# Performance work log

Hardware: AMD Instinct MI355X
Metric: run time of the kernel (lower is better)

## Reference

```python
import jax, jax.numpy as jnp
import numpy as np

NUM_NODES = 100000
EMBED_DIM = 128
NUM_RELATIONS = 64
BATCH = 512


def setup_inputs() -> dict:
    key = jax.random.key(0)
    k1, k2, k3, k4, k5 = jax.random.split(key, 5)
    u = jax.random.randint(k1, (BATCH,), 0, NUM_NODES)
    v = jax.random.randint(k2, (BATCH,), 0, NUM_NODES)
    r = jax.random.randint(k3, (BATCH,), 0, NUM_RELATIONS)
    node_embeddings = jax.random.normal(k4, (NUM_NODES, EMBED_DIM), dtype=jnp.float32)
    relation_matrices = jax.random.normal(k5, (NUM_RELATIONS, EMBED_DIM, EMBED_DIM), dtype=jnp.float32)
    return {"u": u, "v": v, "r": r,
            "node_embeddings": node_embeddings,
            "relation_matrices": relation_matrices}


def reference(u, v, r, node_embeddings, relation_matrices):
    u_embed = node_embeddings[u]            # [B, D]
    v_embed = node_embeddings[v]            # [B, D]
    rel = relation_matrices[r]              # [B, D, D] per-sample gathered matrices
    # torch.matmul([B,D], [B,D,D]) broadcasts u_embed over the relation batch -> [B_rel, B_u, D]
    score = jnp.einsum('ud,bde->bue', u_embed, rel)   # [B, B, D]
    # matmul with v_embed.T [D, B] -> [B, B, B]
    score = jnp.einsum('bue,ve->buv', score, v_embed)  # [B, B, B]
    return jax.nn.sigmoid(score)
```

## Files before the change

kernel.cpp:

```cpp
#include <hip/hip_runtime.h>


#define BATCH 512
#define DIM   128
#define NRELS 64
#define NTHR  256

typedef float floatx4 __attribute__((ext_vector_type(4)));

#define T_ELEMS   ((size_t)NRELS * DIM * BATCH)
#define CNT_OFF   (T_ELEMS)
#define LIST_OFF  (T_ELEMS + 64)
#define WS_NEED   ((T_ELEMS + 64 + (size_t)NRELS * BATCH) * 4)

__global__ __launch_bounds__(NTHR, 2)
void rad_prep_kernel(const int* __restrict__ u_idx,
                     const int* __restrict__ r_idx,
                     const float* __restrict__ nodes,
                     const float* __restrict__ rels,
                     float* __restrict__ ws)
{
    const int bid = (int)blockIdx.x;
    const int t   = (int)threadIdx.x;

    if (bid == NRELS * 8) {
        __shared__ int s_cnt[NRELS];
        int* counts = (int*)(ws + CNT_OFF);
        int* lists  = (int*)(ws + LIST_OFF);
        if (t < NRELS) s_cnt[t] = 0;
        __syncthreads();
        for (int i = t; i < BATCH; i += NTHR) {
            const int rel = r_idx[i];
            const int pos = atomicAdd(&s_cnt[rel], 1);
            lists[rel * BATCH + pos] = i;
        }
        __syncthreads();
        if (t < NRELS) counts[t] = s_cnt[t];
        return;
    }

    const int rel = bid >> 3;
    const int ut0 = (bid & 7) * 64;

    __shared__ __align__(16) float UEsT[DIM * 64];
    __shared__ __align__(16) float Rs[16 * DIM];

    const int tu = t >> 4;
    const int tx = t & 15;

    for (int i = t; i < 64 * (DIM / 4); i += NTHR) {
        const int row = i & 63;
        const int dc  = i >> 6;
        const float4 val = *reinterpret_cast<const float4*>(
            nodes + (size_t)u_idx[ut0 + row] * DIM + dc * 4);
        UEsT[(dc * 4 + 0) * 64 + row] = val.x;
        UEsT[(dc * 4 + 1) * 64 + row] = val.y;
        UEsT[(dc * 4 + 2) * 64 + row] = val.z;
        UEsT[(dc * 4 + 3) * 64 + row] = val.w;
    }

    float accA[4][8];
    #pragma unroll
    for (int i = 0; i < 4; ++i)
        #pragma unroll
        for (int j = 0; j < 8; ++j) accA[i][j] = 0.f;

    const float* Rbase = rels + (size_t)rel * DIM * DIM;
    for (int dch = 0; dch < DIM / 16; ++dch) {
        __syncthreads();
        for (int i = t; i < 16 * (DIM / 4); i += NTHR) {
            const int rr = i >> 5;
            const int cc = i & 31;
            *reinterpret_cast<float4*>(Rs + rr * DIM + cc * 4) =
                *reinterpret_cast<const float4*>(
                    Rbase + (size_t)(dch * 16 + rr) * DIM + cc * 4);
        }
        __syncthreads();
        #pragma unroll
        for (int dd = 0; dd < 16; ++dd) {
            const int d = dch * 16 + dd;
            const float4 a  = *reinterpret_cast<const float4*>(UEsT + d * 64 + tu * 4);
            const float4 b0 = *reinterpret_cast<const float4*>(Rs + dd * DIM + tx * 4);
            const float4 b1 = *reinterpret_cast<const float4*>(Rs + dd * DIM + 64 + tx * 4);
            const float av[4] = {a.x, a.y, a.z, a.w};
            const float bv[8] = {b0.x, b0.y, b0.z, b0.w, b1.x, b1.y, b1.z, b1.w};
            #pragma unroll
            for (int i = 0; i < 4; ++i)
                #pragma unroll
                for (int j = 0; j < 8; ++j)
                    accA[i][j] = fmaf(av[i], bv[j], accA[i][j]);
        }
    }

    #pragma unroll
    for (int j = 0; j < 8; ++j) {
        const int e = (j < 4) ? (tx * 4 + j) : (64 + tx * 4 + (j - 4));
        float4 w4 = make_float4(accA[0][j], accA[1][j], accA[2][j], accA[3][j]);
        *reinterpret_cast<float4*>(
            ws + ((size_t)rel * DIM + e) * BATCH + ut0 + tu * 4) = w4;
    }
}

__global__ __launch_bounds__(NTHR, 2)
void rad_tile_kernel(const int* __restrict__ v_idx,
                     const float* __restrict__ nodes,
                     const float* __restrict__ ws,
                     float* __restrict__ out)
{
    const int bid = (int)blockIdx.x;
    const int rel = bid >> 6;
    const int ut0 = ((bid >> 3) & 7) * 64;
    const int vt0 = (bid & 7) * 64;

    const int* counts = (const int*)(ws + CNT_OFF);
    const int* lists  = (const int*)(ws + LIST_OFF) + rel * BATCH;
    const int  mc     = counts[rel];
    if (mc == 0) return;

    __shared__ __align__(16) float TsT[DIM * 64];
    __shared__ __align__(16) float VEsT[DIM * 64];

    const int t  = (int)threadIdx.x;
    const int tu = t >> 4;
    const int tx = t & 15;

    const float* Tbase = ws + (size_t)rel * DIM * BATCH + ut0;
    for (int i = t; i < DIM * 16; i += NTHR) {
        const int e  = i >> 4;
        const int uc = i & 15;
        *reinterpret_cast<float4*>(TsT + e * 64 + uc * 4) =
            *reinterpret_cast<const float4*>(Tbase + (size_t)e * BATCH + uc * 4);
    }
    for (int i = t; i < 64 * (DIM / 4); i += NTHR) {
        const int row = i & 63;
        const int ec  = i >> 6;
        const float4 val = *reinterpret_cast<const float4*>(
            nodes + (size_t)v_idx[vt0 + row] * DIM + ec * 4);
        VEsT[(ec * 4 + 0) * 64 + row] = val.x;
        VEsT[(ec * 4 + 1) * 64 + row] = val.y;
        VEsT[(ec * 4 + 2) * 64 + row] = val.z;
        VEsT[(ec * 4 + 3) * 64 + row] = val.w;
    }
    __syncthreads();

    float acc[4][4];
    #pragma unroll
    for (int i = 0; i < 4; ++i)
        #pragma unroll
        for (int j = 0; j < 4; ++j) acc[i][j] = 0.f;

    #pragma unroll 8
    for (int e = 0; e < DIM; ++e) {
        const float4 a = *reinterpret_cast<const float4*>(TsT  + e * 64 + tu * 4);
        const float4 b = *reinterpret_cast<const float4*>(VEsT + e * 64 + tx * 4);
        const float av[4] = {a.x, a.y, a.z, a.w};
        const float bv[4] = {b.x, b.y, b.z, b.w};
        #pragma unroll
        for (int i = 0; i < 4; ++i)
            #pragma unroll
            for (int j = 0; j < 4; ++j)
                acc[i][j] = fmaf(av[i], bv[j], acc[i][j]);
    }

    floatx4 sg[4];
    #pragma unroll
    for (int i = 0; i < 4; ++i) {
        sg[i].x = 1.f / (1.f + __expf(-acc[i][0]));
        sg[i].y = 1.f / (1.f + __expf(-acc[i][1]));
        sg[i].z = 1.f / (1.f + __expf(-acc[i][2]));
        sg[i].w = 1.f / (1.f + __expf(-acc[i][3]));
    }

    for (int m = 0; m < mc; ++m) {
        const int bb = lists[m];
        float* obase = out + (size_t)bb * BATCH * BATCH + vt0 + tx * 4;
        #pragma unroll
        for (int i = 0; i < 4; ++i) {
            __builtin_nontemporal_store(
                sg[i], reinterpret_cast<floatx4*>(
                           obase + (size_t)(ut0 + tu * 4 + i) * BATCH));
        }
    }
}

__global__ __launch_bounds__(NTHR, 2)
void rad_fused_kernel(const int* __restrict__ u_idx,
                      const int* __restrict__ v_idx,
                      const int* __restrict__ r_idx,
                      const float* __restrict__ nodes,
                      const float* __restrict__ rels,
                      float* __restrict__ out)
{
    const int rel = (int)blockIdx.x >> 3;
    const int ut0 = ((int)blockIdx.x & 7) * 64;

    __shared__ int s_match[BATCH];
    __shared__ int s_mc;
    __shared__ __align__(16) float s_TsT[DIM * 64];
    __shared__ __align__(16) float s_buf[DIM * 64 + 16 * DIM];

    const int t  = (int)threadIdx.x;
    const int tu = t >> 4;
    const int tx = t & 15;

    if (t == 0) s_mc = 0;
    __syncthreads();
    for (int i = t; i < BATCH; i += NTHR) {
        if (r_idx[i] == rel) {
            int p = atomicAdd(&s_mc, 1);
            s_match[p] = i;
        }
    }

    float* UEsT = s_buf;
    float* Rs   = s_buf + DIM * 64;

    for (int i = t; i < 64 * (DIM / 4); i += NTHR) {
        const int row = i & 63;
        const int dc  = i >> 6;
        const float4 val = *reinterpret_cast<const float4*>(
            nodes + (size_t)u_idx[ut0 + row] * DIM + dc * 4);
        UEsT[(dc * 4 + 0) * 64 + row] = val.x;
        UEsT[(dc * 4 + 1) * 64 + row] = val.y;
        UEsT[(dc * 4 + 2) * 64 + row] = val.z;
        UEsT[(dc * 4 + 3) * 64 + row] = val.w;
    }
    __syncthreads();
    const int mc = s_mc;
    if (mc == 0) return;

    float accA[4][8];
    #pragma unroll
    for (int i = 0; i < 4; ++i)
        #pragma unroll
        for (int j = 0; j < 8; ++j) accA[i][j] = 0.f;

    const float* Rbase = rels + (size_t)rel * DIM * DIM;
    for (int dch = 0; dch < DIM / 16; ++dch) {
        for (int i = t; i < 16 * (DIM / 4); i += NTHR) {
            const int rr = i >> 5;
            const int cc = i & 31;
            *reinterpret_cast<float4*>(Rs + rr * DIM + cc * 4) =
                *reinterpret_cast<const float4*>(
                    Rbase + (size_t)(dch * 16 + rr) * DIM + cc * 4);
        }
        __syncthreads();
        #pragma unroll
        for (int dd = 0; dd < 16; ++dd) {
            const int d = dch * 16 + dd;
            const float4 a  = *reinterpret_cast<const float4*>(UEsT + d * 64 + tu * 4);
            const float4 b0 = *reinterpret_cast<const float4*>(Rs + dd * DIM + tx * 4);
            const float4 b1 = *reinterpret_cast<const float4*>(Rs + dd * DIM + 64 + tx * 4);
            const float av[4] = {a.x, a.y, a.z, a.w};
            const float bv[8] = {b0.x, b0.y, b0.z, b0.w, b1.x, b1.y, b1.z, b1.w};
            #pragma unroll
            for (int i = 0; i < 4; ++i)
                #pragma unroll
                for (int j = 0; j < 8; ++j)
                    accA[i][j] = fmaf(av[i], bv[j], accA[i][j]);
        }
        __syncthreads();
    }

    #pragma unroll
    for (int j = 0; j < 8; ++j) {
        const int e = (j < 4) ? (tx * 4 + j) : (64 + tx * 4 + (j - 4));
        #pragma unroll
        for (int i = 0; i < 4; ++i)
            s_TsT[e * 64 + tu * 4 + i] = accA[i][j];
    }

    float* VEsT = s_buf;
    for (int vt = 0; vt < BATCH / 64; ++vt) {
        __syncthreads();
        for (int i = t; i < 64 * (DIM / 4); i += NTHR) {
            const int row = i & 63;
            const int ec  = i >> 6;
            const float4 val = *reinterpret_cast<const float4*>(
                nodes + (size_t)v_idx[vt * 64 + row] * DIM + ec * 4);
            VEsT[(ec * 4 + 0) * 64 + row] = val.x;
            VEsT[(ec * 4 + 1) * 64 + row] = val.y;
            VEsT[(ec * 4 + 2) * 64 + row] = val.z;
            VEsT[(ec * 4 + 3) * 64 + row] = val.w;
        }
        __syncthreads();

        float acc[4][4];
        #pragma unroll
        for (int i = 0; i < 4; ++i)
            #pragma unroll
            for (int j = 0; j < 4; ++j) acc[i][j] = 0.f;

        #pragma unroll 8
        for (int e = 0; e < DIM; ++e) {
            const float4 a = *reinterpret_cast<const float4*>(s_TsT + e * 64 + tu * 4);
            const float4 b = *reinterpret_cast<const float4*>(VEsT  + e * 64 + tx * 4);
            const float av[4] = {a.x, a.y, a.z, a.w};
            const float bv[4] = {b.x, b.y, b.z, b.w};
            #pragma unroll
            for (int i = 0; i < 4; ++i)
                #pragma unroll
                for (int j = 0; j < 4; ++j)
                    acc[i][j] = fmaf(av[i], bv[j], acc[i][j]);
        }

        floatx4 sg[4];
        #pragma unroll
        for (int i = 0; i < 4; ++i) {
            sg[i].x = 1.f / (1.f + __expf(-acc[i][0]));
            sg[i].y = 1.f / (1.f + __expf(-acc[i][1]));
            sg[i].z = 1.f / (1.f + __expf(-acc[i][2]));
            sg[i].w = 1.f / (1.f + __expf(-acc[i][3]));
        }

        for (int m = 0; m < mc; ++m) {
            const int bb = s_match[m];
            float* obase = out + (size_t)bb * BATCH * BATCH;
            #pragma unroll
            for (int i = 0; i < 4; ++i) {
                floatx4* dst = reinterpret_cast<floatx4*>(
                    obase + (size_t)(ut0 + tu * 4 + i) * BATCH + vt * 64 + tx * 4);
                __builtin_nontemporal_store(sg[i], dst);
            }
        }
    }
}

extern "C" void kernel_launch(void* const* d_in, const int* in_sizes, int n_in,
                              void* d_out, int out_size, void* d_ws, size_t ws_size,
                              hipStream_t stream) {
    const int*   u_idx = (const int*)d_in[0];
    const int*   v_idx = (const int*)d_in[1];
    const int*   r_idx = (const int*)d_in[2];
    const float* nodes = (const float*)d_in[3];
    const float* rels  = (const float*)d_in[4];
    float* out = (float*)d_out;

    if (ws_size >= WS_NEED) {
        float* ws = (float*)d_ws;
        rad_prep_kernel<<<dim3(NRELS * 8 + 1), dim3(NTHR), 0, stream>>>(
            u_idx, r_idx, nodes, rels, ws);
        rad_tile_kernel<<<dim3(NRELS * 8 * 8), dim3(NTHR), 0, stream>>>(
            v_idx, nodes, ws, out);
    } else {
        rad_fused_kernel<<<dim3(NRELS * 8), dim3(NTHR), 0, stream>>>(
            u_idx, v_idx, r_idx, nodes, rels, out);
    }
}
```

Baseline: 154.7 us.

## Swizzle block-to-tile mapping and replace syncthreads with lighter LDS-only barriers

```diff
diff --git a/kernel.cpp b/kernel.cpp
--- a/kernel.cpp
+++ b/kernel.cpp
@@ -108,9 +108,11 @@
                      float* __restrict__ out)
 {
     const int bid = (int)blockIdx.x;
-    const int rel = bid >> 6;
-    const int ut0 = ((bid >> 3) & 7) * 64;
-    const int vt0 = (bid & 7) * 64;
+    const int x   = bid & 7;
+    const int k   = bid >> 3;
+    const int rel = k >> 3;
+    const int vt0 = (k & 7) * 64;
+    const int ut0 = ((x - rel) & 7) * 64;
 
     const int* counts = (const int*)(ws + CNT_OFF);
     const int* lists  = (const int*)(ws + LIST_OFF) + rel * BATCH;
@@ -183,6 +185,12 @@
     }
 }
 
+__device__ __forceinline__ void lds_barrier() {
+    asm volatile("s_waitcnt lgkmcnt(0)" ::: "memory");
+    __builtin_amdgcn_s_barrier();
+    __builtin_amdgcn_sched_barrier(0);
+}
+
 __global__ __launch_bounds__(NTHR, 2)
 void rad_fused_kernel(const int* __restrict__ u_idx,
                       const int* __restrict__ v_idx,
@@ -191,8 +199,9 @@
                       const float* __restrict__ rels,
                       float* __restrict__ out)
 {
-    const int rel = (int)blockIdx.x >> 3;
-    const int ut0 = ((int)blockIdx.x & 7) * 64;
+    const int bid = (int)blockIdx.x;
+    const int rel = ((bid & 7) << 3) | (bid >> 6);
+    const int ut0 = ((bid >> 3) & 7) * 64;
 
     __shared__ int s_match[BATCH];
     __shared__ int s_mc;
@@ -244,7 +253,7 @@
                 *reinterpret_cast<const float4*>(
                     Rbase + (size_t)(dch * 16 + rr) * DIM + cc * 4);
         }
-        __syncthreads();
+        lds_barrier();
         #pragma unroll
         for (int dd = 0; dd < 16; ++dd) {
             const int d = dch * 16 + dd;
@@ -259,7 +268,7 @@
                 for (int j = 0; j < 8; ++j)
                     accA[i][j] = fmaf(av[i], bv[j], accA[i][j]);
         }
-        __syncthreads();
+        lds_barrier();
     }
 
     #pragma unroll
@@ -272,7 +281,7 @@
 
     float* VEsT = s_buf;
     for (int vt = 0; vt < BATCH / 64; ++vt) {
-        __syncthreads();
+        lds_barrier();
         for (int i = t; i < 64 * (DIM / 4); i += NTHR) {
             const int row = i & 63;
             const int ec  = i >> 6;
@@ -283,7 +292,7 @@
             VEsT[(ec * 4 + 2) * 64 + row] = val.z;
             VEsT[(ec * 4 + 3) * 64 + row] = val.w;
         }
-        __syncthreads();
+        lds_barrier();
 
         float acc[4][4];
         #pragma unroll
@@ -315,12 +324,12 @@
 
         for (int m = 0; m < mc; ++m) {
             const int bb = s_match[m];
-            float* obase = out + (size_t)bb * BATCH * BATCH;
+            float* obase = out + (size_t)bb * BATCH * BATCH + vt * 64 + tx * 4;
             #pragma unroll
             for (int i = 0; i < 4; ++i) {
-                floatx4* dst = reinterpret_cast<floatx4*>(
-                    obase + (size_t)(ut0 + tu * 4 + i) * BATCH + vt * 64 + tx * 4);
-                __builtin_nontemporal_store(sg[i], dst);
+                __builtin_nontemporal_store(
+                    sg[i], reinterpret_cast<floatx4*>(
+                               obase + (size_t)(ut0 + tu * 4 + i) * BATCH));
             }
         }
     }
```

Measured after the change: 149.3 us. 1.04x faster.
